# Kernel tuning notes

Measured on AMD Instinct MI355X. Metric: run time of the kernel, lower is better.

## Reference

```python
import jax, jax.numpy as jnp
import numpy as np


def _hippo_dplr(n):
    # HiPPO-LegS -> NPLR -> DPLR (diagonal plus low rank) init, as in S4
    pr = np.sqrt(1.0 + 2.0 * np.arange(n))
    A = -(np.tril(pr[:, None] * pr[None, :]) - np.diag(np.arange(n)))
    p = np.sqrt(np.arange(n) + 0.5)
    b = np.sqrt(2.0 * np.arange(n) + 1.0)
    S = A + p[:, None] * p[None, :]
    lam_re = np.full(n, np.mean(np.diagonal(S)))
    lam_im, V = np.linalg.eigh(S * -1j)  # S*-1j is Hermitian
    p_c = V.conj().T @ p.astype(np.complex128)
    b_c = V.conj().T @ b.astype(np.complex128)
    return lam_re, lam_im, p_c, b_c


def setup_inputs():
    B, L, H, N = 4, 1024, 512, 64
    key = jax.random.key(0)
    kx, kc, ks, k1, k2 = jax.random.split(key, 5)
    lam_re, lam_im, p_c, b_c = _hippo_dplr(N)
    c = jax.random.normal(kc, (N, 2)) * (0.5 ** 0.5)
    f32 = lambda a: jnp.asarray(a, dtype=jnp.float32)
    return {
        'x': jax.random.normal(kx, (B, L, H), dtype=jnp.float32),
        'norm_weight': jnp.ones((H,), jnp.float32),
        'norm_bias': jnp.zeros((H,), jnp.float32),
        'lambda_re': f32(lam_re), 'lambda_im': f32(lam_im),
        'p_re': f32(p_c.real), 'p_im': f32(p_c.imag),
        'b_re': f32(b_c.real), 'b_im': f32(b_c.imag),
        'c_re': c[:, 0].astype(jnp.float32), 'c_im': c[:, 1].astype(jnp.float32),
        'd': jnp.ones((), jnp.float32),
        'log_step': jax.random.uniform(ks, (), jnp.float32, float(np.log(0.001)), float(np.log(0.1))),
        'out_w': (jax.random.normal(k1, (H, H), jnp.float32) / np.sqrt(H)).astype(jnp.float32),
        'out_b': jnp.zeros((H,), jnp.float32),
        'out2_w': (jax.random.normal(k2, (H, H), jnp.float32) / np.sqrt(H)).astype(jnp.float32),
        'out2_b': jnp.zeros((H,), jnp.float32),
    }


def reference(x, norm_weight, norm_bias, lambda_re, lambda_im, p_re, p_im,
              b_re, b_im, c_re, c_im, d, log_step, out_w, out_b, out2_w, out2_b):
    Bsz, L, H = x.shape
    skip = x
    # LayerNorm over channel dim (eps=1e-5, eqx default)
    mu = jnp.mean(x, -1, keepdims=True)
    var = jnp.mean((x - mu) ** 2, -1, keepdims=True)
    xn = (x - mu) / jnp.sqrt(var + 1e-5) * norm_weight + norm_bias
    # --- S4 DPLR bilinear discretization ---
    lam = (lambda_re + 1j * lambda_im).astype(jnp.complex64)
    p = (p_re + 1j * p_im).astype(jnp.complex64)
    b = (b_re + 1j * b_im).astype(jnp.complex64)
    c = (c_re + 1j * c_im).astype(jnp.complex64)
    step = jnp.exp(log_step).astype(jnp.complex64)
    N = lam.shape[0]
    I = jnp.eye(N, dtype=jnp.complex64)
    A = jnp.diag(lam) - p[:, None] * p[None, :].conj()
    A0 = (2.0 / step) * I + A
    Dinv = jnp.diag(1.0 / ((2.0 / step) - lam))
    qcD = p.conj()[None, :] @ Dinv           # [1,N]
    Dp = Dinv @ p[:, None]                   # [N,1]
    A1 = Dinv - (Dp @ qcD) / (1.0 + (qcD @ p[:, None]))  # Woodbury
    Ab = A1 @ A0                             # [N,N] discrete state matrix
    Bb = 2.0 * (A1 @ b[:, None])[:, 0]       # [N]
    # --- sequential state-space scan over time, vectorized over (B,H) lanes ---
    u = xn.astype(jnp.complex64)             # [B,L,H]

    def step_fn(state, u_t):                 # state: [B,H,N], u_t: [B,H]
        new = jnp.einsum('nm,bhm->bhn', Ab, state) + u_t[..., None] * Bb
        return new, jnp.einsum('n,bhn->bh', c, new).real

    init = jnp.zeros((Bsz, H, N), jnp.complex64)
    _, ys = jax.lax.scan(step_fn, init, jnp.moveaxis(u, 1, 0))  # ys: [L,B,H]
    y = jnp.moveaxis(ys, 0, 1) + d * xn      # feedthrough term
    # --- GELU + GLU-style gated output projection, residual ---
    y = jax.nn.gelu(y)
    gate = jax.nn.sigmoid(y @ out2_w.T + out2_b)
    return skip + (y @ out_w.T + out_b) * gate
```

## Files before the change

kernel.cpp:

```cpp
#include <hip/hip_runtime.h>
#include <hip/hip_bf16.h>
#include <math.h>

#define HDIM 512
#define LSEQ 1024
#define BSZ  4

typedef __attribute__((ext_vector_type(8))) short short8;
typedef __attribute__((ext_vector_type(4))) float floatx4;

__device__ __forceinline__ float2 cmul(float2 a, float2 b) {
  float2 r;
  r.x = a.x * b.x - a.y * b.y;
  r.y = a.x * b.y + a.y * b.x;
  return r;
}
__device__ __forceinline__ float2 cadd(float2 a, float2 b) {
  float2 r; r.x = a.x + b.x; r.y = a.y + b.y; return r;
}
__device__ __forceinline__ float2 cfma(float2 a, float2 b, float2 c) {
  c.x += a.x * b.x - a.y * b.y;
  c.y += a.x * b.y + a.y * b.x;
  return c;
}
__device__ __forceinline__ ushort f2bf(float f) {
  __hip_bfloat16 h = __float2bfloat16(f);
  return *(ushort*)&h;
}

__global__ __launch_bounds__(576) void stage1_kernel(
    const float* __restrict__ x, const float* __restrict__ nw,
    const float* __restrict__ nb, float* __restrict__ xn,
    const float* __restrict__ lre, const float* __restrict__ lim,
    const float* __restrict__ pre, const float* __restrict__ pim,
    const float* __restrict__ bre, const float* __restrict__ bim,
    const float* __restrict__ cre, const float* __restrict__ cim,
    const float* __restrict__ logstep, float* __restrict__ Kout) {
  __shared__ float2 Ldab[64], Lu[64], Lr[64], LBb[64];
  __shared__ float2 Rv[2048];
  __shared__ float2 Wv[2048];
  int tid = threadIdx.x;
  int wv = tid >> 6;
  int lane = tid & 63;

  if (blockIdx.x != 0) {
    int row = (blockIdx.x - 1) * 9 + wv;
    if (row >= BSZ * LSEQ) return;
    const float* xr = x + (size_t)row * HDIM;
    float4 v0 = ((const float4*)xr)[lane];
    float4 v1 = ((const float4*)xr)[lane + 64];
    float s  = v0.x + v0.y + v0.z + v0.w + v1.x + v1.y + v1.z + v1.w;
    float ss = v0.x*v0.x + v0.y*v0.y + v0.z*v0.z + v0.w*v0.w
             + v1.x*v1.x + v1.y*v1.y + v1.z*v1.z + v1.w*v1.w;
    #pragma unroll
    for (int m = 1; m < 64; m <<= 1) { s += __shfl_xor(s, m); ss += __shfl_xor(ss, m); }
    float mu   = s * (1.0f / HDIM);
    float var  = ss * (1.0f / HDIM) - mu * mu;
    float rstd = rsqrtf(var + 1e-5f);
    float4 w0 = ((const float4*)nw)[lane];
    float4 w1 = ((const float4*)nw)[lane + 64];
    float4 b0 = ((const float4*)nb)[lane];
    float4 b1 = ((const float4*)nb)[lane + 64];
    float4 o0, o1;
    o0.x = (v0.x - mu) * rstd * w0.x + b0.x;
    o0.y = (v0.y - mu) * rstd * w0.y + b0.y;
    o0.z = (v0.z - mu) * rstd * w0.z + b0.z;
    o0.w = (v0.w - mu) * rstd * w0.w + b0.w;
    o1.x = (v1.x - mu) * rstd * w1.x + b1.x;
    o1.y = (v1.y - mu) * rstd * w1.y + b1.y;
    o1.z = (v1.z - mu) * rstd * w1.z + b1.z;
    o1.w = (v1.w - mu) * rstd * w1.w + b1.w;
    float* xo = xn + (size_t)row * HDIM;
    ((float4*)xo)[lane] = o0;
    ((float4*)xo)[lane + 64] = o1;
    return;
  }

  if (tid < 64) {
    int n = tid;
    float step = expf(logstep[0]);
    float g = 2.0f / step;
    float lr = lre[n], li = lim[n];
    float pr = pre[n], pi = pim[n];
    float br = bre[n], bi = bim[n];
    float den  = (g - lr) * (g - lr) + li * li;
    float dinr = (g - lr) / den, dini = li / den;
    float dabr = (g + lr) * dinr - li * dini;
    float dabi = (g + lr) * dini + li * dinr;
    float ur = dinr * pr - dini * pi;
    float ui = dinr * pi + dini * pr;
    float qr = pr * dinr + pi * dini;
    float qi = pr * dini - pi * dinr;
    float pm2 = pr * pr + pi * pi;
    float betr = pm2 * dinr, beti = pm2 * dini;
    float gar = qr * br - qi * bi;
    float gai = qr * bi + qi * br;
    #pragma unroll
    for (int m = 1; m < 64; m <<= 1) {
      betr += __shfl_xor(betr, m); beti += __shfl_xor(beti, m);
      gar  += __shfl_xor(gar, m);  gai  += __shfl_xor(gai, m);
    }
    float obr = 1.0f + betr, obi = beti;
    float ob2 = obr * obr + obi * obi;
    float kr = -2.0f * g * obr / ob2;
    float ki =  2.0f * g * obi / ob2;
    float rr = kr * qr - ki * qi;
    float ri = kr * qi + ki * qr;
    float tgr = (gar * obr + gai * obi) / ob2;
    float tgi = (gai * obr - gar * obi) / ob2;
    float dbr = dinr * br - dini * bi;
    float dbi = dinr * bi + dini * br;
    float Bbr = 2.0f * (dbr - (ur * tgr - ui * tgi));
    float Bbi = 2.0f * (dbi - (ur * tgi + ui * tgr));
    float2 t;
    t.x = dabr; t.y = dabi; Ldab[n] = t;
    t.x = ur;   t.y = ui;   Lu[n]   = t;
    t.x = rr;   t.y = ri;   Lr[n]   = t;
    t.x = Bbr;  t.y = Bbi;  LBb[n]  = t;
  }
  if (wv == 8) { float2 cc; cc.x = cre[lane]; cc.y = cim[lane]; Rv[lane] = cc; }
  __syncthreads();

  int g8 = lane >> 3;
  int q8 = lane & 7;
  int jm = wv * 8 + g8;
  float2 cv[8];

  if (wv < 8) {
    float2 dab[8], u[8], rn[8];
    #pragma unroll
    for (int ii = 0; ii < 8; ii++) {
      int n = q8 * 8 + ii;
      dab[ii] = Ldab[n]; u[ii] = Lu[n]; rn[ii] = Lr[n];
    }
    float2 rj = Lr[jm];
    #pragma unroll
    for (int ii = 0; ii < 8; ii++) {
      int n = q8 * 8 + ii;
      cv[ii] = cmul(u[ii], rj);
      if (n == jm) cv[ii] = cadd(cv[ii], dab[ii]);
    }
    for (int s = 0; s < 31; s++) {
      float2 part; part.x = 0.f; part.y = 0.f;
      #pragma unroll
      for (int ii = 0; ii < 8; ii++) part = cfma(rn[ii], cv[ii], part);
      #pragma unroll
      for (int m = 1; m < 8; m <<= 1) {
        part.x += __shfl_xor(part.x, m);
        part.y += __shfl_xor(part.y, m);
      }
      #pragma unroll
      for (int ii = 0; ii < 8; ii++) {
        float2 nc = cmul(dab[ii], cv[ii]);
        cv[ii] = cfma(u[ii], part, nc);
      }
    }
  } else {
    float2 dab0 = Ldab[lane], u0 = Lu[lane], r0 = Lr[lane];
    float2 w = LBb[lane];
    Wv[lane * 32 + 0] = w;
    for (int b = 1; b < 32; b++) {
      float dr = r0.x * w.x - r0.y * w.y;
      float di = r0.x * w.y + r0.y * w.x;
      #pragma unroll
      for (int m = 1; m < 64; m <<= 1) { dr += __shfl_xor(dr, m); di += __shfl_xor(di, m); }
      float2 nw2;
      nw2.x = dab0.x * w.x - dab0.y * w.y + u0.x * dr - u0.y * di;
      nw2.y = dab0.x * w.y + dab0.y * w.x + u0.x * di + u0.y * dr;
      w = nw2;
      Wv[lane * 32 + b] = w;
    }
  }
  __syncthreads();

  for (int a = 1; a < 32; a++) {
    if (wv < 8) {
      float2 part; part.x = 0.f; part.y = 0.f;
      #pragma unroll
      for (int ii = 0; ii < 8; ii++) {
        float2 Rk = Rv[(a - 1) * 64 + q8 * 8 + ii];
        part = cfma(Rk, cv[ii], part);
      }
      #pragma unroll
      for (int m = 1; m < 8; m <<= 1) {
        part.x += __shfl_xor(part.x, m);
        part.y += __shfl_xor(part.y, m);
      }
      if (q8 == 0) Rv[a * 64 + jm] = part;
    }
    __syncthreads();
  }

  for (int midx = tid; midx < 1024; midx += 576) {
    int a = midx >> 5, b = midx & 31;
    float acc = 0.f;
    for (int n = 0; n < 64; n++) {
      float2 R = Rv[a * 64 + n];
      float2 W = Wv[n * 32 + b];
      acc += R.x * W.x - R.y * W.y;
    }
    Kout[midx] = acc;
  }
}

__global__ __launch_bounds__(256) void prep_kernel(
    const float* __restrict__ xn, const float* __restrict__ K,
    const float* __restrict__ w1, const float* __restrict__ w2,
    ushort* __restrict__ Uhi, ushort* __restrict__ Ulo,
    ushort* __restrict__ Thi, ushort* __restrict__ Tlo,
    ushort* __restrict__ Wst) {
  __shared__ float tile[64][65];
  int blk = blockIdx.x;
  int tid = threadIdx.x;
  if (blk < 512) {
    int ht = blk & 7, lt = (blk >> 3) & 15, b = blk >> 7;
    #pragma unroll
    for (int q = 0; q < 16; q++) {
      int idx = q * 256 + tid;
      int r = idx >> 6, c = idx & 63;
      tile[r][c] = xn[((size_t)(b * LSEQ + lt * 64 + r)) * HDIM + ht * 64 + c];
    }
    __syncthreads();
    #pragma unroll
    for (int q = 0; q < 16; q++) {
      int idx = q * 256 + tid;
      int r = idx >> 6, c = idx & 63;
      float v = tile[c][r];
      ushort h = f2bf(v);
      float rem = v - __bfloat162float(*(__hip_bfloat16*)&h);
      ushort l = f2bf(rem);
      size_t off = ((size_t)(b * HDIM + ht * 64 + r)) * LSEQ + lt * 64 + c;
      Uhi[off] = h;
      Ulo[off] = l;
    }
  } else if (blk < 768) {
    int e0 = ((blk - 512) * 256 + tid) * 8;
    int n = e0 >> 9, k0 = e0 & 511;
    const float* Wr = (n < 512) ? (w1 + (size_t)n * 512 + k0)
                                : (w2 + (size_t)(n - 512) * 512 + k0);
    ushort tmp[8];
    #pragma unroll
    for (int t = 0; t < 8; t++) tmp[t] = f2bf(Wr[t]);
    *(short8*)&Wst[e0] = *(short8*)tmp;
  } else {
    int r = blk - 768;
    int t = r * 2 + (tid >> 7);
    int tau0 = (tid & 127) * 8;
    ushort hi[8], lo[8];
    #pragma unroll
    for (int q = 0; q < 8; q++) {
      int tau = tau0 + q;
      float v = (tau <= t) ? K[t - tau] : 0.f;
      hi[q] = f2bf(v);
      float rem = v - __bfloat162float(*(__hip_bfloat16*)&hi[q]);
      lo[q] = f2bf(rem);
    }
    *(short8*)&Thi[(size_t)t * 1024 + tau0] = *(short8*)hi;
    *(short8*)&Tlo[(size_t)t * 1024 + tau0] = *(short8*)lo;
  }
}

__global__ __launch_bounds__(256) void conv_gemm_kernel(
    const ushort* __restrict__ Thi, const ushort* __restrict__ Tlo,
    const ushort* __restrict__ Uhi, const ushort* __restrict__ Ulo,
    const float* __restrict__ xn, const float* __restrict__ dptr,
    __hip_bfloat16* __restrict__ A) {
  __shared__ ushort sTh[64 * 40];
  __shared__ ushort sTl[64 * 40];
  __shared__ ushort sUh[64 * 40];
  __shared__ ushort sUl[64 * 40];
  int tid = threadIdx.x;
  int lane = tid & 63;
  int wv = tid >> 6;
  int wm = wv >> 1, wn = wv & 1;
  int by = blockIdx.y;
  int bm = (by < 8) ? by : 23 - by;
  int bn = blockIdx.x;
  floatx4 acc[2][2] = {};
  int srow = tid >> 2;
  int scol = (tid & 3) * 8;
  int fr = lane & 15, fq = (lane >> 4) * 8;
  size_t Toff = (size_t)(bm * 64 + srow) * 1024 + scol;
  size_t Uoff = (size_t)(bn * 64 + srow) * 1024 + scol;
  int KT = 2 * (bm + 1);
  for (int kt = 0; kt < KT; kt++) {
    int k0 = kt * 32;
    *(uint4*)&sTh[srow * 40 + scol] = *(const uint4*)&Thi[Toff + k0];
    *(uint4*)&sTl[srow * 40 + scol] = *(const uint4*)&Tlo[Toff + k0];
    *(uint4*)&sUh[srow * 40 + scol] = *(const uint4*)&Uhi[Uoff + k0];
    *(uint4*)&sUl[srow * 40 + scol] = *(const uint4*)&Ulo[Uoff + k0];
    __syncthreads();
    short8 ah[2], al[2], bh[2], bl[2];
    #pragma unroll
    for (int i = 0; i < 2; i++) {
      ah[i] = *(const short8*)&sTh[(wm * 32 + i * 16 + fr) * 40 + fq];
      al[i] = *(const short8*)&sTl[(wm * 32 + i * 16 + fr) * 40 + fq];
      bh[i] = *(const short8*)&sUh[(wn * 32 + i * 16 + fr) * 40 + fq];
      bl[i] = *(const short8*)&sUl[(wn * 32 + i * 16 + fr) * 40 + fq];
    }
    #pragma unroll
    for (int i = 0; i < 2; i++)
      #pragma unroll
      for (int j = 0; j < 2; j++) {
        acc[i][j] = __builtin_amdgcn_mfma_f32_16x16x32_bf16(ah[i], bh[j], acc[i][j], 0, 0, 0);
        acc[i][j] = __builtin_amdgcn_mfma_f32_16x16x32_bf16(al[i], bh[j], acc[i][j], 0, 0, 0);
        acc[i][j] = __builtin_amdgcn_mfma_f32_16x16x32_bf16(ah[i], bl[j], acc[i][j], 0, 0, 0);
      }
    __syncthreads();
  }
  float d = dptr[0];
  int row0 = bm * 64 + wm * 32;
  int col0 = bn * 64 + wn * 32;
  int fc = lane & 15, frq = (lane >> 4) * 4;
  #pragma unroll
  for (int i = 0; i < 2; i++)
    #pragma unroll
    for (int j = 0; j < 2; j++)
      #pragma unroll
      for (int r = 0; r < 4; r++) {
        int t = row0 + i * 16 + frq + r;
        int c = col0 + j * 16 + fc;
        int b = c >> 9, h = c & 511;
        size_t off = (size_t)(b * LSEQ + t) * HDIM + h;
        float y = acc[i][j][r] + d * xn[off];
        float tnh = tanhf(0.7978845608028654f * (y + 0.044715f * y * y * y));
        A[off] = __float2bfloat16(0.5f * y * (1.0f + tnh));
      }
}

__global__ __launch_bounds__(256) void proj_kernel(
    const __hip_bfloat16* __restrict__ Abuf, const ushort* __restrict__ Wst,
    const float* __restrict__ x, const float* __restrict__ ob,
    const float* __restrict__ o2b, float* __restrict__ out) {
  __shared__ ushort sA[64 * 40];
  __shared__ ushort sW1[64 * 40];
  __shared__ ushort sW2[64 * 40];
  int tid = threadIdx.x;
  int lane = tid & 63;
  int wv = tid >> 6;
  int wm = wv >> 1, wn = wv & 1;
  int bm = blockIdx.y, bn = blockIdx.x;
  int srow = tid >> 2;
  int scol = (tid & 3) * 8;
  int fr = lane & 15, fq = (lane >> 4) * 8;
  floatx4 acc1[2][2] = {}, acc2[2][2] = {};
  const ushort* Ab = (const ushort*)Abuf;
  size_t Aoff  = (size_t)(bm * 64 + srow) * 512 + scol;
  size_t W1off = (size_t)(bn * 64 + srow) * 512 + scol;
  size_t W2off = W1off + (size_t)512 * 512;
  for (int kt = 0; kt < 16; kt++) {
    int k0 = kt * 32;
    *(uint4*)&sA[srow * 40 + scol]  = *(const uint4*)&Ab[Aoff + k0];
    *(uint4*)&sW1[srow * 40 + scol] = *(const uint4*)&Wst[W1off + k0];
    *(uint4*)&sW2[srow * 40 + scol] = *(const uint4*)&Wst[W2off + k0];
    __syncthreads();
    short8 af[2], b1[2], b2[2];
    #pragma unroll
    for (int i = 0; i < 2; i++) {
      af[i] = *(const short8*)&sA[(wm * 32 + i * 16 + fr) * 40 + fq];
      b1[i] = *(const short8*)&sW1[(wn * 32 + i * 16 + fr) * 40 + fq];
      b2[i] = *(const short8*)&sW2[(wn * 32 + i * 16 + fr) * 40 + fq];
    }
    #pragma unroll
    for (int i = 0; i < 2; i++)
      #pragma unroll
      for (int j = 0; j < 2; j++) {
        acc1[i][j] = __builtin_amdgcn_mfma_f32_16x16x32_bf16(af[i], b1[j], acc1[i][j], 0, 0, 0);
        acc2[i][j] = __builtin_amdgcn_mfma_f32_16x16x32_bf16(af[i], b2[j], acc2[i][j], 0, 0, 0);
      }
    __syncthreads();
  }
  int row0 = bm * 64 + wm * 32;
  int col0 = bn * 64 + wn * 32;
  int fc = lane & 15, frq = (lane >> 4) * 4;
  #pragma unroll
  for (int i = 0; i < 2; i++)
    #pragma unroll
    for (int j = 0; j < 2; j++)
      #pragma unroll
      for (int r = 0; r < 4; r++) {
        int row = row0 + i * 16 + frq + r;
        int col = col0 + j * 16 + fc;
        float c1 = acc1[i][j][r] + ob[col];
        float c2 = acc2[i][j][r] + o2b[col];
        float gate = 1.0f / (1.0f + expf(-c2));
        size_t off = (size_t)row * HDIM + col;
        out[off] = x[off] + c1 * gate;
      }
}

extern "C" void kernel_launch(void* const* d_in, const int* in_sizes, int n_in,
                              void* d_out, int out_size, void* d_ws, size_t ws_size,
                              hipStream_t stream) {
  const float* x   = (const float*)d_in[0];
  const float* nw  = (const float*)d_in[1];
  const float* nb  = (const float*)d_in[2];
  const float* lre = (const float*)d_in[3];
  const float* lim = (const float*)d_in[4];
  const float* pre = (const float*)d_in[5];
  const float* pim = (const float*)d_in[6];
  const float* bre = (const float*)d_in[7];
  const float* bim = (const float*)d_in[8];
  const float* cre = (const float*)d_in[9];
  const float* cim = (const float*)d_in[10];
  const float* dsc = (const float*)d_in[11];
  const float* lst = (const float*)d_in[12];
  const float* w1  = (const float*)d_in[13];
  const float* ob  = (const float*)d_in[14];
  const float* w2  = (const float*)d_in[15];
  const float* o2b = (const float*)d_in[16];

  char* ws = (char*)d_ws;
  float* xn    = (float*)(ws);
  ushort* Uhi  = (ushort*)(ws + (size_t)(8  << 20));
  ushort* Ulo  = (ushort*)(ws + (size_t)(12 << 20));
  ushort* Thi  = (ushort*)(ws + (size_t)(16 << 20));
  ushort* Tlo  = (ushort*)(ws + (size_t)(18 << 20));
  ushort* Wst  = (ushort*)(ws + (size_t)(20 << 20));
  __hip_bfloat16* Abuf = (__hip_bfloat16*)(ws + (size_t)(21 << 20));
  float* Kbuf  = (float*)(ws + (size_t)(25 << 20));
  float* out   = (float*)d_out;

  stage1_kernel<<<dim3(457), dim3(576), 0, stream>>>(x, nw, nb, xn,
                                                     lre, lim, pre, pim, bre, bim,
                                                     cre, cim, lst, Kbuf);
  prep_kernel<<<dim3(1280), dim3(256), 0, stream>>>(xn, Kbuf, w1, w2,
                                                    Uhi, Ulo, Thi, Tlo, Wst);
  conv_gemm_kernel<<<dim3(32, 16), dim3(256), 0, stream>>>(Thi, Tlo, Uhi, Ulo,
                                                           xn, dsc, Abuf);
  proj_kernel<<<dim3(8, 64), dim3(256), 0, stream>>>(Abuf, Wst, x, ob, o2b, out);
}
```

Measured before the change: 172.1 us.

## Fuse four kernels into one cooperative persistent kernel with grid syncs

Replaces the four launches (stage1, prep, conv GEMM, projection) with a single cooperative kernel of 256 blocks of 512 threads. Stages are separated by grid.sync. Each block loops over several tiles per stage, and the GEMM stages are reworked with double-buffered shared memory and register prefetch. The goal is to remove launch gaps and tail effects between kernels. The cost is grid-wide barriers and only 256 blocks, so there may be less parallelism and less latency hiding per stage.

```diff
diff --git a/kernel.cpp b/kernel.cpp
--- a/kernel.cpp
+++ b/kernel.cpp
@@ -1,6 +1,9 @@
 #include <hip/hip_runtime.h>
 #include <hip/hip_bf16.h>
+#include <hip/hip_cooperative_groups.h>
 #include <math.h>
+
+namespace cg = cooperative_groups;
 
 #define HDIM 512
 #define LSEQ 1024
@@ -28,106 +31,119 @@
   return *(ushort*)&h;
 }
 
-__global__ __launch_bounds__(576) void stage1_kernel(
-    const float* __restrict__ x, const float* __restrict__ nw,
-    const float* __restrict__ nb, float* __restrict__ xn,
-    const float* __restrict__ lre, const float* __restrict__ lim,
-    const float* __restrict__ pre, const float* __restrict__ pim,
-    const float* __restrict__ bre, const float* __restrict__ bim,
-    const float* __restrict__ cre, const float* __restrict__ cim,
-    const float* __restrict__ logstep, float* __restrict__ Kout) {
-  __shared__ float2 Ldab[64], Lu[64], Lr[64], LBb[64];
-  __shared__ float2 Rv[2048];
-  __shared__ float2 Wv[2048];
-  int tid = threadIdx.x;
-  int wv = tid >> 6;
-  int lane = tid & 63;
-
-  if (blockIdx.x != 0) {
-    int row = (blockIdx.x - 1) * 9 + wv;
-    if (row >= BSZ * LSEQ) return;
-    const float* xr = x + (size_t)row * HDIM;
-    float4 v0 = ((const float4*)xr)[lane];
-    float4 v1 = ((const float4*)xr)[lane + 64];
-    float s  = v0.x + v0.y + v0.z + v0.w + v1.x + v1.y + v1.z + v1.w;
-    float ss = v0.x*v0.x + v0.y*v0.y + v0.z*v0.z + v0.w*v0.w
-             + v1.x*v1.x + v1.y*v1.y + v1.z*v1.z + v1.w*v1.w;
-    #pragma unroll
-    for (int m = 1; m < 64; m <<= 1) { s += __shfl_xor(s, m); ss += __shfl_xor(ss, m); }
-    float mu   = s * (1.0f / HDIM);
-    float var  = ss * (1.0f / HDIM) - mu * mu;
-    float rstd = rsqrtf(var + 1e-5f);
-    float4 w0 = ((const float4*)nw)[lane];
-    float4 w1 = ((const float4*)nw)[lane + 64];
-    float4 b0 = ((const float4*)nb)[lane];
-    float4 b1 = ((const float4*)nb)[lane + 64];
-    float4 o0, o1;
-    o0.x = (v0.x - mu) * rstd * w0.x + b0.x;
-    o0.y = (v0.y - mu) * rstd * w0.y + b0.y;
-    o0.z = (v0.z - mu) * rstd * w0.z + b0.z;
-    o0.w = (v0.w - mu) * rstd * w0.w + b0.w;
-    o1.x = (v1.x - mu) * rstd * w1.x + b1.x;
-    o1.y = (v1.y - mu) * rstd * w1.y + b1.y;
-    o1.z = (v1.z - mu) * rstd * w1.z + b1.z;
-    o1.w = (v1.w - mu) * rstd * w1.w + b1.w;
-    float* xo = xn + (size_t)row * HDIM;
-    ((float4*)xo)[lane] = o0;
-    ((float4*)xo)[lane + 64] = o1;
-    return;
-  }
-
-  if (tid < 64) {
-    int n = tid;
-    float step = expf(logstep[0]);
-    float g = 2.0f / step;
-    float lr = lre[n], li = lim[n];
-    float pr = pre[n], pi = pim[n];
-    float br = bre[n], bi = bim[n];
-    float den  = (g - lr) * (g - lr) + li * li;
-    float dinr = (g - lr) / den, dini = li / den;
-    float dabr = (g + lr) * dinr - li * dini;
-    float dabi = (g + lr) * dini + li * dinr;
-    float ur = dinr * pr - dini * pi;
-    float ui = dinr * pi + dini * pr;
-    float qr = pr * dinr + pi * dini;
-    float qi = pr * dini - pi * dinr;
-    float pm2 = pr * pr + pi * pi;
-    float betr = pm2 * dinr, beti = pm2 * dini;
-    float gar = qr * br - qi * bi;
-    float gai = qr * bi + qi * br;
-    #pragma unroll
-    for (int m = 1; m < 64; m <<= 1) {
-      betr += __shfl_xor(betr, m); beti += __shfl_xor(beti, m);
-      gar  += __shfl_xor(gar, m);  gai  += __shfl_xor(gai, m);
-    }
-    float obr = 1.0f + betr, obi = beti;
-    float ob2 = obr * obr + obi * obi;
-    float kr = -2.0f * g * obr / ob2;
-    float ki =  2.0f * g * obi / ob2;
-    float rr = kr * qr - ki * qi;
-    float ri = kr * qi + ki * qr;
-    float tgr = (gar * obr + gai * obi) / ob2;
-    float tgi = (gai * obr - gar * obi) / ob2;
-    float dbr = dinr * br - dini * bi;
-    float dbi = dinr * bi + dini * br;
-    float Bbr = 2.0f * (dbr - (ur * tgr - ui * tgi));
-    float Bbi = 2.0f * (dbi - (ur * tgi + ui * tgr));
-    float2 t;
-    t.x = dabr; t.y = dabi; Ldab[n] = t;
-    t.x = ur;   t.y = ui;   Lu[n]   = t;
-    t.x = rr;   t.y = ri;   Lr[n]   = t;
-    t.x = Bbr;  t.y = Bbi;  LBb[n]  = t;
-  }
-  if (wv == 8) { float2 cc; cc.x = cre[lane]; cc.y = cim[lane]; Rv[lane] = cc; }
-  __syncthreads();
-
-  int g8 = lane >> 3;
-  int q8 = lane & 7;
-  int jm = wv * 8 + g8;
-  float2 cv[8];
-
-  if (wv < 8) {
-    float2 dab[8], u[8], rn[8];
+struct FusedParams {
+  const float *x, *nw, *nb;
+  const float *lre, *lim, *pre, *pim, *bre, *bim, *cre, *cim, *dsc, *lst;
+  const float *w1, *ob, *w2, *o2b;
+  float* xn;
+  ushort *Uhi, *Ulo, *Thi, *Tlo, *Wst;
+  __hip_bfloat16* Abuf;
+  float* Kbuf;
+  float* out;
+};
+
+__global__ __launch_bounds__(512, 2) void fused_kernel(FusedParams p) {
+  __shared__ __align__(16) char smem[40960];
+  cg::grid_group grid = cg::this_grid();
+  const int tid = threadIdx.x;
+  const int wv = tid >> 6, lane = tid & 63;
+  const int blk = blockIdx.x;
+
+  if (blk < 255) {
+    for (int row = blk * 8 + wv; row < BSZ * LSEQ; row += 2040) {
+      const float* xr = p.x + (size_t)row * HDIM;
+      float4 v0 = ((const float4*)xr)[lane];
+      float4 v1 = ((const float4*)xr)[lane + 64];
+      float s  = v0.x + v0.y + v0.z + v0.w + v1.x + v1.y + v1.z + v1.w;
+      float ss = v0.x*v0.x + v0.y*v0.y + v0.z*v0.z + v0.w*v0.w
+               + v1.x*v1.x + v1.y*v1.y + v1.z*v1.z + v1.w*v1.w;
+      #pragma unroll
+      for (int m = 1; m < 64; m <<= 1) { s += __shfl_xor(s, m); ss += __shfl_xor(ss, m); }
+      float mu   = s * (1.0f / HDIM);
+      float var  = ss * (1.0f / HDIM) - mu * mu;
+      float rstd = rsqrtf(var + 1e-5f);
+      float4 w0 = ((const float4*)p.nw)[lane];
+      float4 w1 = ((const float4*)p.nw)[lane + 64];
+      float4 b0 = ((const float4*)p.nb)[lane];
+      float4 b1 = ((const float4*)p.nb)[lane + 64];
+      float4 o0, o1;
+      o0.x = (v0.x - mu) * rstd * w0.x + b0.x;
+      o0.y = (v0.y - mu) * rstd * w0.y + b0.y;
+      o0.z = (v0.z - mu) * rstd * w0.z + b0.z;
+      o0.w = (v0.w - mu) * rstd * w0.w + b0.w;
+      o1.x = (v1.x - mu) * rstd * w1.x + b1.x;
+      o1.y = (v1.y - mu) * rstd * w1.y + b1.y;
+      o1.z = (v1.z - mu) * rstd * w1.z + b1.z;
+      o1.w = (v1.w - mu) * rstd * w1.w + b1.w;
+      float* xo = p.xn + (size_t)row * HDIM;
+      ((float4*)xo)[lane] = o0;
+      ((float4*)xo)[lane + 64] = o1;
+    }
+    int idx = blk * 512 + tid;
+    if (idx < 65536) {
+      int e0 = idx * 8;
+      int n = e0 >> 9, k0 = e0 & 511;
+      const float* Wr = (n < 512) ? (p.w1 + (size_t)n * 512 + k0)
+                                  : (p.w2 + (size_t)(n - 512) * 512 + k0);
+      ushort tmp[8];
+      #pragma unroll
+      for (int q = 0; q < 8; q++) tmp[q] = f2bf(Wr[q]);
+      *(short8*)&p.Wst[e0] = *(short8*)tmp;
+    }
+  } else {
+    float2* Ldab = (float2*)smem;
+    float2* Lu  = Ldab + 64;
+    float2* Lr  = Lu + 64;
+    float2* LBb = Lr + 64;
+    float2* Rv  = LBb + 64;
+    float2* Wv  = Rv + 2048;
+    if (tid < 64) {
+      int n = tid;
+      float step = expf(p.lst[0]);
+      float g = 2.0f / step;
+      float lr = p.lre[n], li = p.lim[n];
+      float pr = p.pre[n], pi = p.pim[n];
+      float br = p.bre[n], bi = p.bim[n];
+      float den  = (g - lr) * (g - lr) + li * li;
+      float dinr = (g - lr) / den, dini = li / den;
+      float dabr = (g + lr) * dinr - li * dini;
+      float dabi = (g + lr) * dini + li * dinr;
+      float ur = dinr * pr - dini * pi;
+      float ui = dinr * pi + dini * pr;
+      float qr = pr * dinr + pi * dini;
+      float qi = pr * dini - pi * dinr;
+      float pm2 = pr * pr + pi * pi;
+      float betr = pm2 * dinr, beti = pm2 * dini;
+      float gar = qr * br - qi * bi;
+      float gai = qr * bi + qi * br;
+      #pragma unroll
+      for (int m = 1; m < 64; m <<= 1) {
+        betr += __shfl_xor(betr, m); beti += __shfl_xor(beti, m);
+        gar  += __shfl_xor(gar, m);  gai  += __shfl_xor(gai, m);
+      }
+      float obr = 1.0f + betr, obi = beti;
+      float ob2 = obr * obr + obi * obi;
+      float kr = -2.0f * g * obr / ob2;
+      float ki =  2.0f * g * obi / ob2;
+      float rr = kr * qr - ki * qi;
+      float ri = kr * qi + ki * qr;
+      float tgr = (gar * obr + gai * obi) / ob2;
+      float tgi = (gai * obr - gar * obi) / ob2;
+      float dbr = dinr * br - dini * bi;
+      float dbi = dinr * bi + dini * br;
+      float Bbr = 2.0f * (dbr - (ur * tgr - ui * tgi));
+      float Bbi = 2.0f * (dbi - (ur * tgi + ui * tgr));
+      float2 t;
+      t.x = dabr; t.y = dabi; Ldab[n] = t;
+      t.x = ur;   t.y = ui;   Lu[n]   = t;
+      t.x = rr;   t.y = ri;   Lr[n]   = t;
+      t.x = Bbr;  t.y = Bbi;  LBb[n]  = t;
+    }
+    if (wv == 1) { float2 cc; cc.x = p.cre[lane]; cc.y = p.cim[lane]; Rv[lane] = cc; }
+    __syncthreads();
+    int g8 = lane >> 3, q8 = lane & 7;
+    int jm = wv * 8 + g8;
+    float2 dab[8], u[8], rn[8], cv[8];
     #pragma unroll
     for (int ii = 0; ii < 8; ii++) {
       int n = q8 * 8 + ii;
@@ -155,26 +171,24 @@
         cv[ii] = cfma(u[ii], part, nc);
       }
     }
-  } else {
-    float2 dab0 = Ldab[lane], u0 = Lu[lane], r0 = Lr[lane];
-    float2 w = LBb[lane];
-    Wv[lane * 32 + 0] = w;
-    for (int b = 1; b < 32; b++) {
-      float dr = r0.x * w.x - r0.y * w.y;
-      float di = r0.x * w.y + r0.y * w.x;
-      #pragma unroll
-      for (int m = 1; m < 64; m <<= 1) { dr += __shfl_xor(dr, m); di += __shfl_xor(di, m); }
-      float2 nw2;
-      nw2.x = dab0.x * w.x - dab0.y * w.y + u0.x * dr - u0.y * di;
-      nw2.y = dab0.x * w.y + dab0.y * w.x + u0.x * di + u0.y * dr;
-      w = nw2;
-      Wv[lane * 32 + b] = w;
-    }
-  }
-  __syncthreads();
-
-  for (int a = 1; a < 32; a++) {
-    if (wv < 8) {
+    if (wv == 0) {
+      float2 dab0 = Ldab[lane], u0 = Lu[lane], r0 = Lr[lane];
+      float2 w = LBb[lane];
+      Wv[lane * 32 + 0] = w;
+      for (int b = 1; b < 32; b++) {
+        float dr = r0.x * w.x - r0.y * w.y;
+        float di = r0.x * w.y + r0.y * w.x;
+        #pragma unroll
+        for (int m = 1; m < 64; m <<= 1) { dr += __shfl_xor(dr, m); di += __shfl_xor(di, m); }
+        float2 nw2;
+        nw2.x = dab0.x * w.x - dab0.y * w.y + u0.x * dr - u0.y * di;
+        nw2.y = dab0.x * w.y + dab0.y * w.x + u0.x * di + u0.y * dr;
+        w = nw2;
+        Wv[lane * 32 + b] = w;
+      }
+    }
+    __syncthreads();
+    for (int a = 1; a < 32; a++) {
       float2 part; part.x = 0.f; part.y = 0.f;
       #pragma unroll
       for (int ii = 0; ii < 8; ii++) {
@@ -187,246 +201,247 @@
         part.y += __shfl_xor(part.y, m);
       }
       if (q8 == 0) Rv[a * 64 + jm] = part;
-    }
-    __syncthreads();
+      __syncthreads();
+    }
+    for (int midx = tid; midx < 1024; midx += 512) {
+      int a = midx >> 5, b = midx & 31;
+      float acc = 0.f;
+      for (int n = 0; n < 64; n++) {
+        float2 R = Rv[a * 64 + n];
+        float2 W = Wv[n * 32 + b];
+        acc += R.x * W.x - R.y * W.y;
+      }
+      p.Kbuf[midx] = acc;
+    }
   }
-
-  for (int midx = tid; midx < 1024; midx += 576) {
-    int a = midx >> 5, b = midx & 31;
-    float acc = 0.f;
-    for (int n = 0; n < 64; n++) {
-      float2 R = Rv[a * 64 + n];
-      float2 W = Wv[n * 32 + b];
-      acc += R.x * W.x - R.y * W.y;
-    }
-    Kout[midx] = acc;
-  }
-}
-
-__global__ __launch_bounds__(256) void prep_kernel(
-    const float* __restrict__ xn, const float* __restrict__ K,
-    const float* __restrict__ w1, const float* __restrict__ w2,
-    ushort* __restrict__ Uhi, ushort* __restrict__ Ulo,
-    ushort* __restrict__ Thi, ushort* __restrict__ Tlo,
-    ushort* __restrict__ Wst) {
-  __shared__ float tile[64][65];
-  int blk = blockIdx.x;
-  int tid = threadIdx.x;
-  if (blk < 512) {
-    int ht = blk & 7, lt = (blk >> 3) & 15, b = blk >> 7;
+  __threadfence();
+  grid.sync();
+
+  {
+    float (*tile)[65] = (float (*)[65])smem;
     #pragma unroll
-    for (int q = 0; q < 16; q++) {
-      int idx = q * 256 + tid;
-      int r = idx >> 6, c = idx & 63;
-      tile[r][c] = xn[((size_t)(b * LSEQ + lt * 64 + r)) * HDIM + ht * 64 + c];
-    }
-    __syncthreads();
-    #pragma unroll
-    for (int q = 0; q < 16; q++) {
-      int idx = q * 256 + tid;
-      int r = idx >> 6, c = idx & 63;
-      float v = tile[c][r];
-      ushort h = f2bf(v);
-      float rem = v - __bfloat162float(*(__hip_bfloat16*)&h);
-      ushort l = f2bf(rem);
-      size_t off = ((size_t)(b * HDIM + ht * 64 + r)) * LSEQ + lt * 64 + c;
-      Uhi[off] = h;
-      Ulo[off] = l;
-    }
-  } else if (blk < 768) {
-    int e0 = ((blk - 512) * 256 + tid) * 8;
-    int n = e0 >> 9, k0 = e0 & 511;
-    const float* Wr = (n < 512) ? (w1 + (size_t)n * 512 + k0)
-                                : (w2 + (size_t)(n - 512) * 512 + k0);
-    ushort tmp[8];
-    #pragma unroll
-    for (int t = 0; t < 8; t++) tmp[t] = f2bf(Wr[t]);
-    *(short8*)&Wst[e0] = *(short8*)tmp;
-  } else {
-    int r = blk - 768;
-    int t = r * 2 + (tid >> 7);
+    for (int s2 = 0; s2 < 2; s2++) {
+      int tt = blk * 2 + s2;
+      int ht = tt & 7, lt = (tt >> 3) & 15, b = tt >> 7;
+      #pragma unroll
+      for (int q = 0; q < 8; q++) {
+        int idx = q * 512 + tid;
+        int r = idx >> 6, c = idx & 63;
+        tile[r][c] = p.xn[((size_t)(b * LSEQ + lt * 64 + r)) * HDIM + ht * 64 + c];
+      }
+      __syncthreads();
+      #pragma unroll
+      for (int q = 0; q < 8; q++) {
+        int idx = q * 512 + tid;
+        int r = idx >> 6, c = idx & 63;
+        float v = tile[c][r];
+        ushort h = f2bf(v);
+        float rem = v - __bfloat162float(*(__hip_bfloat16*)&h);
+        ushort l = f2bf(rem);
+        size_t off = ((size_t)(b * HDIM + ht * 64 + r)) * LSEQ + lt * 64 + c;
+        p.Uhi[off] = h;
+        p.Ulo[off] = l;
+      }
+      __syncthreads();
+    }
+    int t = blk * 4 + (tid >> 7);
     int tau0 = (tid & 127) * 8;
     ushort hi[8], lo[8];
     #pragma unroll
     for (int q = 0; q < 8; q++) {
       int tau = tau0 + q;
-      float v = (tau <= t) ? K[t - tau] : 0.f;
+      float v = (tau <= t) ? p.Kbuf[t - tau] : 0.f;
       hi[q] = f2bf(v);
       float rem = v - __bfloat162float(*(__hip_bfloat16*)&hi[q]);
       lo[q] = f2bf(rem);
     }
-    *(short8*)&Thi[(size_t)t * 1024 + tau0] = *(short8*)hi;
-    *(short8*)&Tlo[(size_t)t * 1024 + tau0] = *(short8*)lo;
+    *(short8*)&p.Thi[(size_t)t * 1024 + tau0] = *(short8*)hi;
+    *(short8*)&p.Tlo[(size_t)t * 1024 + tau0] = *(short8*)lo;
   }
-}
-
-__global__ __launch_bounds__(256) void conv_gemm_kernel(
-    const ushort* __restrict__ Thi, const ushort* __restrict__ Tlo,
-    const ushort* __restrict__ Uhi, const ushort* __restrict__ Ulo,
-    const float* __restrict__ xn, const float* __restrict__ dptr,
-    __hip_bfloat16* __restrict__ A) {
-  __shared__ ushort sTh[64 * 40];
-  __shared__ ushort sTl[64 * 40];
-  __shared__ ushort sUh[64 * 40];
-  __shared__ ushort sUl[64 * 40];
-  int tid = threadIdx.x;
-  int lane = tid & 63;
-  int wv = tid >> 6;
-  int wm = wv >> 1, wn = wv & 1;
-  int by = blockIdx.y;
-  int bm = (by < 8) ? by : 23 - by;
-  int bn = blockIdx.x;
-  floatx4 acc[2][2] = {};
-  int srow = tid >> 2;
-  int scol = (tid & 3) * 8;
-  int fr = lane & 15, fq = (lane >> 4) * 8;
-  size_t Toff = (size_t)(bm * 64 + srow) * 1024 + scol;
-  size_t Uoff = (size_t)(bn * 64 + srow) * 1024 + scol;
-  int KT = 2 * (bm + 1);
-  for (int kt = 0; kt < KT; kt++) {
-    int k0 = kt * 32;
-    *(uint4*)&sTh[srow * 40 + scol] = *(const uint4*)&Thi[Toff + k0];
-    *(uint4*)&sTl[srow * 40 + scol] = *(const uint4*)&Tlo[Toff + k0];
-    *(uint4*)&sUh[srow * 40 + scol] = *(const uint4*)&Uhi[Uoff + k0];
-    *(uint4*)&sUl[srow * 40 + scol] = *(const uint4*)&Ulo[Uoff + k0];
-    __syncthreads();
-    short8 ah[2], al[2], bh[2], bl[2];
-    #pragma unroll
-    for (int i = 0; i < 2; i++) {
-      ah[i] = *(const short8*)&sTh[(wm * 32 + i * 16 + fr) * 40 + fq];
-      al[i] = *(const short8*)&sTl[(wm * 32 + i * 16 + fr) * 40 + fq];
-      bh[i] = *(const short8*)&sUh[(wn * 32 + i * 16 + fr) * 40 + fq];
-      bl[i] = *(const short8*)&sUl[(wn * 32 + i * 16 + fr) * 40 + fq];
-    }
-    #pragma unroll
-    for (int i = 0; i < 2; i++)
-      #pragma unroll
-      for (int j = 0; j < 2; j++) {
-        acc[i][j] = __builtin_amdgcn_mfma_f32_16x16x32_bf16(ah[i], bh[j], acc[i][j], 0, 0, 0);
-        acc[i][j] = __builtin_amdgcn_mfma_f32_16x16x32_bf16(al[i], bh[j], acc[i][j], 0, 0, 0);
-        acc[i][j] = __builtin_amdgcn_mfma_f32_16x16x32_bf16(ah[i], bl[j], acc[i][j], 0, 0, 0);
-      }
-    __syncthreads();
+  __threadfence();
+  grid.sync();
+
+  {
+    ushort* sbase = (ushort*)smem;
+    const int wm = wv >> 1, wn = wv & 1;
+    const int fr = lane & 15, fq = (lane >> 4) * 8;
+    const int fc = lane & 15, frq = (lane >> 4) * 4;
+    const int bm0 = blk >> 5, bn = blk & 31;
+    const float d = p.dsc[0];
+    const int si = tid & 255;
+    const int srow = si >> 2, scol = (si & 3) * 8;
+    const int ldst = (tid < 256 ? 0 : 5120) + srow * 40 + scol;
+    #pragma unroll 1
+    for (int tp = 0; tp < 2; tp++) {
+      const int bm = tp ? 15 - bm0 : bm0;
+      const int KT = 2 * (bm + 1);
+      const ushort *g0, *g1;
+      size_t Goff;
+      if (tid < 256) { g0 = p.Thi; g1 = p.Tlo; Goff = (size_t)(bm * 64 + srow) * 1024 + scol; }
+      else           { g0 = p.Uhi; g1 = p.Ulo; Goff = (size_t)(bn * 64 + srow) * 1024 + scol; }
+      uint4 c0 = *(const uint4*)&g0[Goff];
+      uint4 c1 = *(const uint4*)&g1[Goff];
+      *(uint4*)&sbase[ldst]        = c0;
+      *(uint4*)&sbase[ldst + 2560] = c1;
+      __syncthreads();
+      floatx4 acc[2] = {};
+      for (int kt = 0; kt < KT; kt++) {
+        const int cur = kt & 1;
+        uint4 n0 = {}, n1 = {};
+        if (kt + 1 < KT) {
+          n0 = *(const uint4*)&g0[Goff + (size_t)(kt + 1) * 32];
+          n1 = *(const uint4*)&g1[Goff + (size_t)(kt + 1) * 32];
+        }
+        const ushort* sTh = sbase + cur * 10240;
+        const ushort* sTl = sTh + 2560;
+        const ushort* sUh = sTh + 5120;
+        const ushort* sUl = sTh + 7680;
+        short8 ah  = *(const short8*)&sTh[(wm * 16 + fr) * 40 + fq];
+        short8 al  = *(const short8*)&sTl[(wm * 16 + fr) * 40 + fq];
+        short8 bh0 = *(const short8*)&sUh[(wn * 32 + fr) * 40 + fq];
+        short8 bh1 = *(const short8*)&sUh[(wn * 32 + 16 + fr) * 40 + fq];
+        short8 bl0 = *(const short8*)&sUl[(wn * 32 + fr) * 40 + fq];
+        short8 bl1 = *(const short8*)&sUl[(wn * 32 + 16 + fr) * 40 + fq];
+        acc[0] = __builtin_amdgcn_mfma_f32_16x16x32_bf16(ah, bh0, acc[0], 0, 0, 0);
+        acc[0] = __builtin_amdgcn_mfma_f32_16x16x32_bf16(al, bh0, acc[0], 0, 0, 0);
+        acc[0] = __builtin_amdgcn_mfma_f32_16x16x32_bf16(ah, bl0, acc[0], 0, 0, 0);
+        acc[1] = __builtin_amdgcn_mfma_f32_16x16x32_bf16(ah, bh1, acc[1], 0, 0, 0);
+        acc[1] = __builtin_amdgcn_mfma_f32_16x16x32_bf16(al, bh1, acc[1], 0, 0, 0);
+        acc[1] = __builtin_amdgcn_mfma_f32_16x16x32_bf16(ah, bl1, acc[1], 0, 0, 0);
+        if (kt + 1 < KT) {
+          ushort* dst = sbase + (cur ^ 1) * 10240;
+          *(uint4*)&dst[ldst]        = n0;
+          *(uint4*)&dst[ldst + 2560] = n1;
+        }
+        __syncthreads();
+      }
+      const int row0 = bm * 64 + wm * 16;
+      const int col0 = bn * 64 + wn * 32;
+      #pragma unroll
+      for (int j = 0; j < 2; j++)
+        #pragma unroll
+        for (int r = 0; r < 4; r++) {
+          int t = row0 + frq + r;
+          int c = col0 + j * 16 + fc;
+          int b = c >> 9, h = c & 511;
+          size_t off = (size_t)(b * LSEQ + t) * HDIM + h;
+          float y = acc[j][r] + d * p.xn[off];
+          float tnh = tanhf(0.7978845608028654f * (y + 0.044715f * y * y * y));
+          p.Abuf[off] = __float2bfloat16(0.5f * y * (1.0f + tnh));
+        }
+    }
   }
-  float d = dptr[0];
-  int row0 = bm * 64 + wm * 32;
-  int col0 = bn * 64 + wn * 32;
-  int fc = lane & 15, frq = (lane >> 4) * 4;
-  #pragma unroll
-  for (int i = 0; i < 2; i++)
-    #pragma unroll
-    for (int j = 0; j < 2; j++)
-      #pragma unroll
-      for (int r = 0; r < 4; r++) {
-        int t = row0 + i * 16 + frq + r;
-        int c = col0 + j * 16 + fc;
-        int b = c >> 9, h = c & 511;
-        size_t off = (size_t)(b * LSEQ + t) * HDIM + h;
-        float y = acc[i][j][r] + d * xn[off];
-        float tnh = tanhf(0.7978845608028654f * (y + 0.044715f * y * y * y));
-        A[off] = __float2bfloat16(0.5f * y * (1.0f + tnh));
-      }
-}
-
-__global__ __launch_bounds__(256) void proj_kernel(
-    const __hip_bfloat16* __restrict__ Abuf, const ushort* __restrict__ Wst,
-    const float* __restrict__ x, const float* __restrict__ ob,
-    const float* __restrict__ o2b, float* __restrict__ out) {
-  __shared__ ushort sA[64 * 40];
-  __shared__ ushort sW1[64 * 40];
-  __shared__ ushort sW2[64 * 40];
-  int tid = threadIdx.x;
-  int lane = tid & 63;
-  int wv = tid >> 6;
-  int wm = wv >> 1, wn = wv & 1;
-  int bm = blockIdx.y, bn = blockIdx.x;
-  int srow = tid >> 2;
-  int scol = (tid & 3) * 8;
-  int fr = lane & 15, fq = (lane >> 4) * 8;
-  floatx4 acc1[2][2] = {}, acc2[2][2] = {};
-  const ushort* Ab = (const ushort*)Abuf;
-  size_t Aoff  = (size_t)(bm * 64 + srow) * 512 + scol;
-  size_t W1off = (size_t)(bn * 64 + srow) * 512 + scol;
-  size_t W2off = W1off + (size_t)512 * 512;
-  for (int kt = 0; kt < 16; kt++) {
-    int k0 = kt * 32;
-    *(uint4*)&sA[srow * 40 + scol]  = *(const uint4*)&Ab[Aoff + k0];
-    *(uint4*)&sW1[srow * 40 + scol] = *(const uint4*)&Wst[W1off + k0];
-    *(uint4*)&sW2[srow * 40 + scol] = *(const uint4*)&Wst[W2off + k0];
-    __syncthreads();
-    short8 af[2], b1[2], b2[2];
-    #pragma unroll
-    for (int i = 0; i < 2; i++) {
-      af[i] = *(const short8*)&sA[(wm * 32 + i * 16 + fr) * 40 + fq];
-      b1[i] = *(const short8*)&sW1[(wn * 32 + i * 16 + fr) * 40 + fq];
-      b2[i] = *(const short8*)&sW2[(wn * 32 + i * 16 + fr) * 40 + fq];
-    }
-    #pragma unroll
-    for (int i = 0; i < 2; i++)
-      #pragma unroll
-      for (int j = 0; j < 2; j++) {
-        acc1[i][j] = __builtin_amdgcn_mfma_f32_16x16x32_bf16(af[i], b1[j], acc1[i][j], 0, 0, 0);
-        acc2[i][j] = __builtin_amdgcn_mfma_f32_16x16x32_bf16(af[i], b2[j], acc2[i][j], 0, 0, 0);
-      }
-    __syncthreads();
+  __threadfence();
+  grid.sync();
+
+  {
+    ushort* sbase = (ushort*)smem;
+    const int wm = wv >> 1, wn = wv & 1;
+    const int fr = lane & 15, fq = (lane >> 4) * 8;
+    const int fc = lane & 15, frq = (lane >> 4) * 4;
+    const int si = tid & 255;
+    const int srow = si >> 2, scol = (si & 3) * 8;
+    const ushort* Ab = (const ushort*)p.Abuf;
+    #pragma unroll 1
+    for (int tp = 0; tp < 2; tp++) {
+      const int tt = blk + tp * 256;
+      const int bm = tt >> 3, bn = tt & 7;
+      size_t Aoff  = (size_t)(bm * 64 + srow) * 512 + scol;
+      size_t W1off = (size_t)(bn * 64 + srow) * 512 + scol;
+      size_t W2off = (size_t)(512 + bn * 64 + srow) * 512 + scol;
+      if (tid < 256) {
+        *(uint4*)&sbase[srow * 40 + scol]        = *(const uint4*)&Ab[Aoff];
+        *(uint4*)&sbase[5120 + srow * 40 + scol] = *(const uint4*)&p.Wst[W2off];
+      } else {
+        *(uint4*)&sbase[2560 + srow * 40 + scol] = *(const uint4*)&p.Wst[W1off];
+      }
+      __syncthreads();
+      floatx4 acc1[2] = {}, acc2[2] = {};
+      for (int kt = 0; kt < 16; kt++) {
+        const int cur = kt & 1;
+        uint4 na = {}, nwa = {};
+        if (kt + 1 < 16) {
+          if (tid < 256) {
+            na  = *(const uint4*)&Ab[Aoff + (kt + 1) * 32];
+            nwa = *(const uint4*)&p.Wst[W2off + (kt + 1) * 32];
+          } else {
+            nwa = *(const uint4*)&p.Wst[W1off + (kt + 1) * 32];
+          }
+        }
+        const ushort* sA  = sbase + cur * 7680;
+        const ushort* sW1 = sA + 2560;
+        const ushort* sW2 = sA + 5120;
+        short8 af  = *(const short8*)&sA[(wm * 16 + fr) * 40 + fq];
+        short8 b10 = *(const short8*)&sW1[(wn * 32 + fr) * 40 + fq];
+        short8 b11 = *(const short8*)&sW1[(wn * 32 + 16 + fr) * 40 + fq];
+        short8 b20 = *(const short8*)&sW2[(wn * 32 + fr) * 40 + fq];
+        short8 b21 = *(const short8*)&sW2[(wn * 32 + 16 + fr) * 40 + fq];
+        acc1[0] = __builtin_amdgcn_mfma_f32_16x16x32_bf16(af, b10, acc1[0], 0, 0, 0);
+        acc1[1] = __builtin_amdgcn_mfma_f32_16x16x32_bf16(af, b11, acc1[1], 0, 0, 0);
+        acc2[0] = __builtin_amdgcn_mfma_f32_16x16x32_bf16(af, b20, acc2[0], 0, 0, 0);
+        acc2[1] = __builtin_amdgcn_mfma_f32_16x16x32_bf16(af, b21, acc2[1], 0, 0, 0);
+        if (kt + 1 < 16) {
+          ushort* dst = sbase + (cur ^ 1) * 7680;
+          if (tid < 256) {
+            *(uint4*)&dst[srow * 40 + scol]        = na;
+            *(uint4*)&dst[5120 + srow * 40 + scol] = nwa;
+          } else {
+            *(uint4*)&dst[2560 + srow * 40 + scol] = nwa;
+          }
+        }
+        __syncthreads();
+      }
+      const int row0 = bm * 64 + wm * 16;
+      const int col0 = bn * 64 + wn * 32;
+      #pragma unroll
+      for (int j = 0; j < 2; j++)
+        #pragma unroll
+        for (int r = 0; r < 4; r++) {
+          int row = row0 + frq + r;
+          int col = col0 + j * 16 + fc;
+          float c1 = acc1[j][r] + p.ob[col];
+          float c2 = acc2[j][r] + p.o2b[col];
+          float gate = 1.0f / (1.0f + expf(-c2));
+          size_t off = (size_t)row * HDIM + col;
+          p.out[off] = p.x[off] + c1 * gate;
+        }
+    }
   }
-  int row0 = bm * 64 + wm * 32;
-  int col0 = bn * 64 + wn * 32;
-  int fc = lane & 15, frq = (lane >> 4) * 4;
-  #pragma unroll
-  for (int i = 0; i < 2; i++)
-    #pragma unroll
-    for (int j = 0; j < 2; j++)
-      #pragma unroll
-      for (int r = 0; r < 4; r++) {
-        int row = row0 + i * 16 + frq + r;
-        int col = col0 + j * 16 + fc;
-        float c1 = acc1[i][j][r] + ob[col];
-        float c2 = acc2[i][j][r] + o2b[col];
-        float gate = 1.0f / (1.0f + expf(-c2));
-        size_t off = (size_t)row * HDIM + col;
-        out[off] = x[off] + c1 * gate;
-      }
 }
 
 extern "C" void kernel_launch(void* const* d_in, const int* in_sizes, int n_in,
                               void* d_out, int out_size, void* d_ws, size_t ws_size,
                               hipStream_t stream) {
-  const float* x   = (const float*)d_in[0];
-  const float* nw  = (const float*)d_in[1];
-  const float* nb  = (const float*)d_in[2];
-  const float* lre = (const float*)d_in[3];
-  const float* lim = (const float*)d_in[4];
-  const float* pre = (const float*)d_in[5];
-  const float* pim = (const float*)d_in[6];
-  const float* bre = (const float*)d_in[7];
-  const float* bim = (const float*)d_in[8];
-  const float* cre = (const float*)d_in[9];
-  const float* cim = (const float*)d_in[10];
-  const float* dsc = (const float*)d_in[11];
-  const float* lst = (const float*)d_in[12];
-  const float* w1  = (const float*)d_in[13];
-  const float* ob  = (const float*)d_in[14];
-  const float* w2  = (const float*)d_in[15];
-  const float* o2b = (const float*)d_in[16];
-
   char* ws = (char*)d_ws;
-  float* xn    = (float*)(ws);
-  ushort* Uhi  = (ushort*)(ws + (size_t)(8  << 20));
-  ushort* Ulo  = (ushort*)(ws + (size_t)(12 << 20));
-  ushort* Thi  = (ushort*)(ws + (size_t)(16 << 20));
-  ushort* Tlo  = (ushort*)(ws + (size_t)(18 << 20));
-  ushort* Wst  = (ushort*)(ws + (size_t)(20 << 20));
-  __hip_bfloat16* Abuf = (__hip_bfloat16*)(ws + (size_t)(21 << 20));
-  float* Kbuf  = (float*)(ws + (size_t)(25 << 20));
-  float* out   = (float*)d_out;
-
-  stage1_kernel<<<dim3(457), dim3(576), 0, stream>>>(x, nw, nb, xn,
-                                                     lre, lim, pre, pim, bre, bim,
-                                                     cre, cim, lst, Kbuf);
-  prep_kernel<<<dim3(1280), dim3(256), 0, stream>>>(xn, Kbuf, w1, w2,
-                                                    Uhi, Ulo, Thi, Tlo, Wst);
-  conv_gemm_kernel<<<dim3(32, 16), dim3(256), 0, stream>>>(Thi, Tlo, Uhi, Ulo,
-                                                           xn, dsc, Abuf);
-  proj_kernel<<<dim3(8, 64), dim3(256), 0, stream>>>(Abuf, Wst, x, ob, o2b, out);
-}
+  FusedParams p;
+  p.x   = (const float*)d_in[0];
+  p.nw  = (const float*)d_in[1];
+  p.nb  = (const float*)d_in[2];
+  p.lre = (const float*)d_in[3];
+  p.lim = (const float*)d_in[4];
+  p.pre = (const float*)d_in[5];
+  p.pim = (const float*)d_in[6];
+  p.bre = (const float*)d_in[7];
+  p.bim = (const float*)d_in[8];
+  p.cre = (const float*)d_in[9];
+  p.cim = (const float*)d_in[10];
+  p.dsc = (const float*)d_in[11];
+  p.lst = (const float*)d_in[12];
+  p.w1  = (const float*)d_in[13];
+  p.ob  = (const float*)d_in[14];
+  p.w2  = (const float*)d_in[15];
+  p.o2b = (const float*)d_in[16];
+  p.xn   = (float*)(ws);
+  p.Uhi  = (ushort*)(ws + (size_t)(8  << 20));
+  p.Ulo  = (ushort*)(ws + (size_t)(12 << 20));
+  p.Thi  = (ushort*)(ws + (size_t)(16 << 20));
+  p.Tlo  = (ushort*)(ws + (size_t)(18 << 20));
+  p.Wst  = (ushort*)(ws + (size_t)(20 << 20));
+  p.Abuf = (__hip_bfloat16*)(ws + (size_t)(21 << 20));
+  p.Kbuf = (float*)(ws + (size_t)(25 << 20));
+  p.out  = (float*)d_out;
+
+  void* args[] = { &p };
+  hipLaunchCooperativeKernel(reinterpret_cast<void*>(fused_kernel),
+                             dim3(256), dim3(512), args, 0, stream);
+}
```

Result: slower. 407.0 us (+136.5%).
